# Kernel optimization log

Hardware: AMD Instinct MI355X
Metric: run time of the kernel (lower is better)

Reference implementation:

```python
import jax, jax.numpy as jnp
import numpy as np

EPS = 1e-7  # tf.keras.backend.epsilon()
R_ITER = 3

def squash(v, axis=-1):
    # Eq.(1): scale = |s|^2 / (1+|s|^2) / |s|
    s2 = jnp.sum(v * v, axis=axis, keepdims=True)
    scale = s2 / (1.0 + s2) / jnp.sqrt(s2 + EPS)
    return scale * v

def setup_inputs() -> dict:
    key = jax.random.key(0)
    k1, k2 = jax.random.split(key)
    B, Ni, Di = 64, 1152, 8
    No, Do = 64, 16
    inputs = jax.random.normal(k1, (B, Ni, Di), dtype=jnp.float32)
    # W init: tf.random.normal(stddev=0.1)
    W = 0.1 * jax.random.normal(k2, (1, Ni, No, Do, Di), dtype=jnp.float32)
    return {"inputs": inputs, "W": W}

def reference(inputs, W):
    B, Ni, Di = inputs.shape
    No, Do = W.shape[2], W.shape[3]
    # inputs_hat[b,i,o,d] = W[i,o,d,k] @ inputs[b,i,k]  (tile+matmul fused)
    u_hat = jnp.einsum('iodk,bik->biod', W[0], inputs)  # [B,Ni,No,Do]
    # raw routing logits start at shape [1,Ni,No]; broadcast to [B,...] on first update
    b_logits = jnp.zeros((1, Ni, No), dtype=inputs.dtype)
    for it in range(R_ITER):
        c = jax.nn.softmax(b_logits, axis=2)            # over output caps
        s = jnp.sum(c[..., None] * u_hat, axis=1, keepdims=True)  # [B,1,No,Do]
        v = squash(s, axis=-1)                          # [B,1,No,Do]
        if it < R_ITER - 1:
            # agreement: <u_hat, v> over capsule dim
            b_logits = b_logits + jnp.sum(u_hat * v, axis=-1)  # [B,Ni,No]
    out = jnp.squeeze(v, axis=1)                        # [B,No,Do]
    routing_weights = c[..., None, None]                # [B,Ni,No,1,1] as in TF
    return out, routing_weights
```

## Files before the change

kernel.cpp:

```cpp
#include <hip/hip_runtime.h>


#define B_      64
#define NI_     1152
#define DI_     8
#define NO_     64
#define DO_     16
#define NOD_    1024
#define CH_     96
#define CI_     12
#define BG_     8
#define BSPLIT_ 8
#define V_ELEMS 65536
#define PADR    33
#define XBSTRIDE 36864

static_assert(CH_ * CI_ == NI_, "chunking");
static_assert(BG_ * BSPLIT_ == B_, "b split");

typedef __attribute__((ext_vector_type(8))) float f8v;

template <int MODE>
__global__ __launch_bounds__(256, 3)
void caps_pass(const float* __restrict__ X,
               const float* __restrict__ W,
               const float* __restrict__ vin,
               float* __restrict__ part,
               float* __restrict__ rw)
{
    __shared__ float4 wtile[NO_ * PADR];
    __shared__ float  e_lds[BG_][NO_];
    __shared__ float  invS[BG_];

    const int t  = threadIdx.x;
    const int o  = t >> 2, q = t & 3;
    const int ch = blockIdx.x;
    const int by = blockIdx.y;
    const int b0 = by * BG_;
    const int i0 = ch * CI_;

    const int phase = ch % CI_;

    float vreg[BG_][4];
    if (MODE >= 1) {
#pragma unroll
        for (int b = 0; b < BG_; ++b) {
            float4 qv = *((const float4*)(vin + (size_t)(b0 + b) * NOD_ + 4 * t));
            vreg[b][0]=qv.x; vreg[b][1]=qv.y; vreg[b][2]=qv.z; vreg[b][3]=qv.w;
        }
    }

    float acc[BG_][4];
#pragma unroll
    for (int b = 0; b < BG_; ++b) { acc[b][0]=0.f; acc[b][1]=0.f; acc[b][2]=0.f; acc[b][3]=0.f; }

    const float4* Wq = (const float4*)W;

    int ci = phase;
    for (int cc = 0; cc < CI_; ++cc) {
        const int i = i0 + ci;

        const float4* wg = Wq + (size_t)i * 2048;
        float4 tmp[8];
#pragma unroll
        for (int j = 0; j < 8; ++j) tmp[j] = wg[t + 256 * j];
#pragma unroll
        for (int j = 0; j < 8; ++j) {
            const int f = t + 256 * j;
            wtile[(f >> 5) * PADR + (f & 31)] = tmp[j];
        }
        __syncthreads();

        float wf[4][8];
#pragma unroll
        for (int jj = 0; jj < 4; ++jj) {
            float4 a0 = wtile[o * PADR + (4 * q + jj) * 2];
            float4 a1 = wtile[o * PADR + (4 * q + jj) * 2 + 1];
            wf[jj][0]=a0.x; wf[jj][1]=a0.y; wf[jj][2]=a0.z; wf[jj][3]=a0.w;
            wf[jj][4]=a1.x; wf[jj][5]=a1.y; wf[jj][6]=a1.z; wf[jj][7]=a1.w;
        }

        f8v xs0, xs1, xs2, xs3, xs4, xs5, xs6, xs7;
        {
            const float* xp  = X + ((size_t)b0 * NI_ + i) * DI_;
            const float* xp4 = xp + 4 * (size_t)NI_ * DI_;
            asm volatile(
                "s_load_dwordx8 %0, %8, 0\n\t"
                "s_load_dwordx8 %1, %8, 36864\n\t"
                "s_load_dwordx8 %2, %8, 73728\n\t"
                "s_load_dwordx8 %3, %8, 110592\n\t"
                "s_load_dwordx8 %4, %9, 0\n\t"
                "s_load_dwordx8 %5, %9, 36864\n\t"
                "s_load_dwordx8 %6, %9, 73728\n\t"
                "s_load_dwordx8 %7, %9, 110592\n\t"
                "s_waitcnt lgkmcnt(0)"
                : "=&s"(xs0), "=&s"(xs1), "=&s"(xs2), "=&s"(xs3),
                  "=&s"(xs4), "=&s"(xs5), "=&s"(xs6), "=&s"(xs7)
                : "s"(xp), "s"(xp4)
                : "memory");
        }

        float u[BG_][4];
#pragma unroll
        for (int b = 0; b < BG_; ++b) {
            const f8v xv = (b==0)?xs0:(b==1)?xs1:(b==2)?xs2:(b==3)?xs3
                         :(b==4)?xs4:(b==5)?xs5:(b==6)?xs6:xs7;
#pragma unroll
            for (int jj = 0; jj < 4; ++jj) {
                float s = wf[jj][0] * xv[0];
                s = fmaf(wf[jj][1], xv[1], s); s = fmaf(wf[jj][2], xv[2], s);
                s = fmaf(wf[jj][3], xv[3], s); s = fmaf(wf[jj][4], xv[4], s);
                s = fmaf(wf[jj][5], xv[5], s); s = fmaf(wf[jj][6], xv[6], s);
                s = fmaf(wf[jj][7], xv[7], s);
                u[b][jj] = s;
            }
            if (MODE >= 1) {
                float a = u[b][0]*vreg[b][0] + u[b][1]*vreg[b][1]
                        + u[b][2]*vreg[b][2] + u[b][3]*vreg[b][3];
                a += __shfl_xor(a, 1);
                a += __shfl_xor(a, 2);
                if (q == 0) e_lds[b][o] = __expf(a);
            } else {
                acc[b][0]+=u[b][0]; acc[b][1]+=u[b][1];
                acc[b][2]+=u[b][2]; acc[b][3]+=u[b][3];
            }
        }

        if (MODE >= 1) {
            __syncthreads();
            {
                const int bb = t >> 5, l = t & 31;
                float s = e_lds[bb][l] + e_lds[bb][l + 32];
                s += __shfl_xor(s, 1);  s += __shfl_xor(s, 2);  s += __shfl_xor(s, 4);
                s += __shfl_xor(s, 8);  s += __shfl_xor(s, 16);
                if (l == 0) invS[bb] = 1.0f / s;
            }
            __syncthreads();
#pragma unroll
            for (int b = 0; b < BG_; ++b) {
                const float c = e_lds[b][o] * invS[b];
                acc[b][0] = fmaf(c, u[b][0], acc[b][0]);
                acc[b][1] = fmaf(c, u[b][1], acc[b][1]);
                acc[b][2] = fmaf(c, u[b][2], acc[b][2]);
                acc[b][3] = fmaf(c, u[b][3], acc[b][3]);
                if (MODE == 2 && q == 0)
                    rw[((size_t)(b0 + b) * NI_ + i) * NO_ + o] = c;
            }
        } else {
            __syncthreads();
        }

        ci = (ci + 1 == CI_) ? 0 : ci + 1;
    }

#pragma unroll
    for (int b = 0; b < BG_; ++b) {
        float4 val;
        val.x=acc[b][0]; val.y=acc[b][1]; val.z=acc[b][2]; val.w=acc[b][3];
        *((float4*)(part + (((size_t)(b0 + b) * CH_ + ch) * NOD_ + 4 * t))) = val;
    }
}

template <int MODE>
__global__ __launch_bounds__(128)
void caps_squash(const float* __restrict__ part, const float* __restrict__ v0in,
                 float* __restrict__ vout)
{
    const int c4 = blockIdx.x * 128 + threadIdx.x;
    const int b = c4 >> 8, od4 = c4 & 255;
    const float4* p = (const float4*)part + (size_t)b * CH_ * 256 + od4;
    float4 s = {0.f, 0.f, 0.f, 0.f};
#pragma unroll 8
    for (int ch = 0; ch < CH_; ++ch) {
        float4 q = p[(size_t)ch * 256];
        s.x += q.x; s.y += q.y; s.z += q.z; s.w += q.w;
    }
    if (MODE == 0) { s.x*=(1.f/64.f); s.y*=(1.f/64.f); s.z*=(1.f/64.f); s.w*=(1.f/64.f); }
    float s2 = s.x*s.x + s.y*s.y + s.z*s.z + s.w*s.w;
    s2 += __shfl_xor(s2, 1); s2 += __shfl_xor(s2, 2);
    const float scale = s2 / ((1.0f + s2) * sqrtf(s2 + 1e-7f));
    float4 v; v.x = scale*s.x; v.y = scale*s.y; v.z = scale*s.z; v.w = scale*s.w;
    if (MODE == 1) {
        float4 v0 = ((const float4*)v0in)[c4];
        v.x += v0.x; v.y += v0.y; v.z += v0.z; v.w += v0.w;
    }
    ((float4*)vout)[c4] = v;
}

__global__ __launch_bounds__(1024, 1)
void caps_naive(const float* __restrict__ X, const float* __restrict__ W,
                float* __restrict__ outv, float* __restrict__ outc)
{
    __shared__ float xs[NI_ * DI_];
    __shared__ float agree[NO_];
    __shared__ float expo[NO_];
    __shared__ float s2sh[NO_];
    __shared__ float den;

    const int b = blockIdx.x, tid = threadIdx.x;
    const int o = tid >> 4, d = tid & 15;

    for (int f = tid; f < NI_ * DI_; f += 1024)
        xs[f] = X[(size_t)b * NI_ * DI_ + f];
    __syncthreads();

    float vprev = 0.f, v0 = 0.f, vout = 0.f;
    for (int phase = 0; phase < 3; ++phase) {
        float sacc = 0.f;
        for (int i = 0; i < NI_; ++i) {
            const float* wp = W + (size_t)i * 8192 + (size_t)tid * 8;
            const float* xp = xs + i * DI_;
            float u = 0.f;
#pragma unroll
            for (int k = 0; k < 8; ++k) u = fmaf(wp[k], xp[k], u);
            if (phase == 0) { sacc += u; continue; }
            if (d == 0) agree[o] = 0.f;
            __syncthreads();
            atomicAdd(&agree[o], u * vprev);
            __syncthreads();
            if (tid == 0) den = 0.f;
            __syncthreads();
            if (d == 0) { float e = __expf(agree[o]); expo[o] = e; atomicAdd(&den, e); }
            __syncthreads();
            float c = expo[o] / den;
            sacc = fmaf(c, u, sacc);
            if (phase == 2 && d == 0)
                outc[((size_t)b * NI_ + i) * NO_ + o] = c;
            __syncthreads();
        }
        if (phase == 0) sacc *= (1.0f / 64.0f);
        if (d == 0) s2sh[o] = 0.f;
        __syncthreads();
        atomicAdd(&s2sh[o], sacc * sacc);
        __syncthreads();
        const float s2 = s2sh[o];
        const float scale = s2 / ((1.0f + s2) * sqrtf(s2 + 1e-7f));
        const float vv = scale * sacc;
        if (phase == 0)      { v0 = vv; vprev = vv; }
        else if (phase == 1) { vprev = v0 + vv; }
        else                 { vout = vv; }
        __syncthreads();
    }
    outv[(size_t)b * (NO_ * DO_) + tid] = vout;
}

extern "C" void kernel_launch(void* const* d_in, const int* in_sizes, int n_in,
                              void* d_out, int out_size, void* d_ws, size_t ws_size,
                              hipStream_t stream)
{
    const float *X, *W;
    if (in_sizes[0] < in_sizes[1]) { X = (const float*)d_in[0]; W = (const float*)d_in[1]; }
    else                           { X = (const float*)d_in[1]; W = (const float*)d_in[0]; }

    float* out  = (float*)d_out;
    float* outv = out;
    float* outc = out + V_ELEMS;

    const size_t needBig = ((size_t)B_ * CH_ * NOD_ + 2 * (size_t)B_ * NOD_) * sizeof(float);
    if (ws_size < needBig) {
        caps_naive<<<B_, 1024, 0, stream>>>(X, W, outv, outc);
        return;
    }

    float* part = (float*)d_ws;
    float* v0   = part + (size_t)B_ * CH_ * NOD_;
    float* w01  = v0 + (size_t)B_ * NOD_;

    dim3 gP(CH_, BSPLIT_), blk(256), gS(128), blkS(128);
    caps_pass<0><<<gP, blk, 0, stream>>>(X, W, nullptr, part, nullptr);
    caps_squash<0><<<gS, blkS, 0, stream>>>(part, nullptr, v0);
    caps_pass<1><<<gP, blk, 0, stream>>>(X, W, v0, part, nullptr);
    caps_squash<1><<<gS, blkS, 0, stream>>>(part, v0, w01);
    caps_pass<2><<<gP, blk, 0, stream>>>(X, W, w01, part, outc);
    caps_squash<2><<<gS, blkS, 0, stream>>>(part, nullptr, outv);
}
```

Before: 220.7 us.

## Prefetch next W tile into registers and split squash reduction across four lanes

The routing pass now loads the next input capsule's W slice into registers right after the current slice is written to shared memory, so global loads overlap the compute of the current iteration. The squash kernel splits the 96-chunk partial-sum reduction across four lanes per output vector and combines them with shuffles, which gives four times as many threads to hide load latency. The prefetch keeps eight float4 values live across the loop body, which raises register pressure at a launch bound of three blocks per CU.

```diff
diff --git a/kernel.cpp b/kernel.cpp
--- a/kernel.cpp
+++ b/kernel.cpp
@@ -13,7 +13,6 @@
 #define BSPLIT_ 8
 #define V_ELEMS 65536
 #define PADR    33
-#define XBSTRIDE 36864
 
 static_assert(CH_ * CI_ == NI_, "chunking");
 static_assert(BG_ * BSPLIT_ == B_, "b split");
@@ -41,6 +40,17 @@
 
     const int phase = ch % CI_;
 
+    const float4* Wq = (const float4*)W;
+
+    int ci = phase;
+
+    float4 tmp[8];
+    {
+        const float4* wg = Wq + (size_t)(i0 + ci) * 2048;
+#pragma unroll
+        for (int j = 0; j < 8; ++j) tmp[j] = wg[t + 256 * j];
+    }
+
     float vreg[BG_][4];
     if (MODE >= 1) {
 #pragma unroll
@@ -54,22 +64,22 @@
 #pragma unroll
     for (int b = 0; b < BG_; ++b) { acc[b][0]=0.f; acc[b][1]=0.f; acc[b][2]=0.f; acc[b][3]=0.f; }
 
-    const float4* Wq = (const float4*)W;
-
-    int ci = phase;
     for (int cc = 0; cc < CI_; ++cc) {
         const int i = i0 + ci;
 
-        const float4* wg = Wq + (size_t)i * 2048;
-        float4 tmp[8];
-#pragma unroll
-        for (int j = 0; j < 8; ++j) tmp[j] = wg[t + 256 * j];
 #pragma unroll
         for (int j = 0; j < 8; ++j) {
             const int f = t + 256 * j;
             wtile[(f >> 5) * PADR + (f & 31)] = tmp[j];
         }
         __syncthreads();
+
+        const int cin = (ci + 1 == CI_) ? 0 : ci + 1;
+        if (cc + 1 < CI_) {
+            const float4* wg = Wq + (size_t)(i0 + cin) * 2048;
+#pragma unroll
+            for (int j = 0; j < 8; ++j) tmp[j] = wg[t + 256 * j];
+        }
 
         float wf[4][8];
 #pragma unroll
@@ -150,7 +160,7 @@
             __syncthreads();
         }
 
-        ci = (ci + 1 == CI_) ? 0 : ci + 1;
+        ci = cin;
     }
 
 #pragma unroll
@@ -162,29 +172,37 @@
 }
 
 template <int MODE>
-__global__ __launch_bounds__(128)
+__global__ __launch_bounds__(256)
 void caps_squash(const float* __restrict__ part, const float* __restrict__ v0in,
                  float* __restrict__ vout)
 {
-    const int c4 = blockIdx.x * 128 + threadIdx.x;
+    const int t  = threadIdx.x;
+    const int li = t >> 2, g = t & 3;
+    const int c4 = blockIdx.x * 64 + li;
     const int b = c4 >> 8, od4 = c4 & 255;
-    const float4* p = (const float4*)part + (size_t)b * CH_ * 256 + od4;
+    const float4* p = (const float4*)part + ((size_t)b * CH_ + (size_t)g * 24) * 256 + od4;
     float4 s = {0.f, 0.f, 0.f, 0.f};
-#pragma unroll 8
-    for (int ch = 0; ch < CH_; ++ch) {
-        float4 q = p[(size_t)ch * 256];
-        s.x += q.x; s.y += q.y; s.z += q.z; s.w += q.w;
-    }
+#pragma unroll
+    for (int cc = 0; cc < 24; ++cc) {
+        float4 qv = p[(size_t)cc * 256];
+        s.x += qv.x; s.y += qv.y; s.z += qv.z; s.w += qv.w;
+    }
+    s.x += __shfl_xor(s.x, 1); s.y += __shfl_xor(s.y, 1);
+    s.z += __shfl_xor(s.z, 1); s.w += __shfl_xor(s.w, 1);
+    s.x += __shfl_xor(s.x, 2); s.y += __shfl_xor(s.y, 2);
+    s.z += __shfl_xor(s.z, 2); s.w += __shfl_xor(s.w, 2);
     if (MODE == 0) { s.x*=(1.f/64.f); s.y*=(1.f/64.f); s.z*=(1.f/64.f); s.w*=(1.f/64.f); }
     float s2 = s.x*s.x + s.y*s.y + s.z*s.z + s.w*s.w;
-    s2 += __shfl_xor(s2, 1); s2 += __shfl_xor(s2, 2);
+    s2 += __shfl_xor(s2, 4); s2 += __shfl_xor(s2, 8);
     const float scale = s2 / ((1.0f + s2) * sqrtf(s2 + 1e-7f));
-    float4 v; v.x = scale*s.x; v.y = scale*s.y; v.z = scale*s.z; v.w = scale*s.w;
-    if (MODE == 1) {
-        float4 v0 = ((const float4*)v0in)[c4];
-        v.x += v0.x; v.y += v0.y; v.z += v0.z; v.w += v0.w;
-    }
-    ((float4*)vout)[c4] = v;
+    if (g == 0) {
+        float4 v; v.x = scale*s.x; v.y = scale*s.y; v.z = scale*s.z; v.w = scale*s.w;
+        if (MODE == 1) {
+            float4 v0 = ((const float4*)v0in)[c4];
+            v.x += v0.x; v.y += v0.y; v.z += v0.z; v.w += v0.w;
+        }
+        ((float4*)vout)[c4] = v;
+    }
 }
 
 __global__ __launch_bounds__(1024, 1)
@@ -266,7 +284,7 @@
     float* v0   = part + (size_t)B_ * CH_ * NOD_;
     float* w01  = v0 + (size_t)B_ * NOD_;
 
-    dim3 gP(CH_, BSPLIT_), blk(256), gS(128), blkS(128);
+    dim3 gP(CH_, BSPLIT_), blk(256), gS(256), blkS(256);
     caps_pass<0><<<gP, blk, 0, stream>>>(X, W, nullptr, part, nullptr);
     caps_squash<0><<<gS, blkS, 0, stream>>>(part, nullptr, v0);
     caps_pass<1><<<gP, blk, 0, stream>>>(X, W, v0, part, nullptr);
```

Result: slower. 402.8 us (+82.5%).
